# Kernel tuning notes

Measured on AMD Instinct MI355X. Metric: run time of the kernel, lower is better.

## Reference

```python
import jax, jax.numpy as jnp
import numpy as np

NU, NB, NI = 50000, 20000, 100000
D = 64
NUM_LAYERS = 2
CORE_K = 3
PAD = NI  # padding index for bundle_items
BATCH, NCAND = 2048, 2
MAXDEG = 50
E_UB, E_UI, E_BI = 800000, 1000000, 1200000
N_UB, N_UI, N_BI = NU + NB, NU + NI, NB + NI


def setup_inputs():
    key = jax.random.key(0)
    ks = jax.random.split(key, 24)
    f = jnp.float32
    inp = {
        'users_feature': jax.random.normal(ks[0], (NU, D), f) * 0.1,
        'bundles_feature': jax.random.normal(ks[1], (NB, D), f) * 0.1,
        'items_feature': jax.random.normal(ks[2], (NI, D), f) * 0.1,
        'mlp_core_w1': jax.random.normal(ks[3], (2, 32), f) * 0.1,
        'mlp_core_b1': jnp.zeros((32,), f),
        'mlp_core_w2': jax.random.normal(ks[4], (32, 1), f) * 0.1,
        'mlp_core_b2': jnp.zeros((1,), f),
        'mlp_syn_w1': jax.random.normal(ks[5], (2 * D, D), f) * 0.05,
        'mlp_syn_b1': jnp.zeros((D,), f),
        'mlp_syn_w2': jax.random.normal(ks[6], (D, D), f) * 0.05,
        'mlp_syn_b2': jnp.zeros((D,), f),
        'ub_val': jax.random.uniform(ks[7], (E_UB,), f) * 0.2,
        'ui_val': jax.random.uniform(ks[8], (E_UI,), f) * 0.2,
        'bi_val': jax.random.uniform(ks[9], (E_BI,), f) * 0.2,
        'users': jax.random.randint(ks[10], (BATCH,), 0, NU),
        'bundles': jax.random.randint(ks[11], (BATCH, NCAND), 0, NB),
        'ub_row': jax.random.randint(ks[12], (E_UB,), 0, N_UB, jnp.int32),
        'ub_col': jax.random.randint(ks[13], (E_UB,), 0, N_UB, jnp.int32),
        'ui_row': jax.random.randint(ks[14], (E_UI,), 0, N_UI, jnp.int32),
        'ui_col': jax.random.randint(ks[15], (E_UI,), 0, N_UI, jnp.int32),
        'bi_row': jax.random.randint(ks[16], (E_BI,), 0, N_BI, jnp.int32),
        'bi_col': jax.random.randint(ks[17], (E_BI,), 0, N_BI, jnp.int32),
        'bundle_items': jax.random.randint(ks[18], (NB, MAXDEG), 0, NI + 1),
    }
    return inp


def spmm(row, col, val, x):
    # y = A @ x for COO sparse A: gather source rows, scale, scatter-add to dest rows
    return jax.ops.segment_sum(val[:, None] * x[col], row, num_segments=x.shape[0])


def propagate(row, col, val, feat_a, feat_b):
    f = jnp.concatenate([feat_a, feat_b], axis=0)
    acc = f
    for _ in range(NUM_LAYERS):
        f = spmm(row, col, val, f)
        acc = acc + f
    m = acc / (NUM_LAYERS + 1)  # mean over hop outputs
    return m[:feat_a.shape[0]], m[feat_a.shape[0]:]


def core_fringe_scores(users, bundles, reps, bundle_items,
                       cw1, cb1, cw2, cb2, sw1, sb1, sw2, sb2):
    UB_u, UB_b, UI_u, UI_i, BI_b, BI_i = reps
    B, C = bundles.shape
    users_exp = jnp.repeat(users, C)            # [B*C]
    bundles_flat = bundles.reshape(-1)          # [B*C]
    bbi = bundle_items[bundles_flat]            # [B*C, M]
    mask = bbi != PAD
    zero = jnp.zeros((1, D), UI_i.dtype)
    items_ui = jnp.concatenate([UI_i, zero], 0)[bbi]  # [B*C, M, D]
    items_bi = jnp.concatenate([BI_i, zero], 0)[bbi]
    u_ui = UI_u[users_exp]                      # [B*C, D]
    b_bi = BI_b[bundles_flat]
    r_UI = jnp.einsum('nd,nmd->nm', u_ui, items_ui)
    r_BI = jnp.einsum('nd,nmd->nm', b_bi, items_bi)
    x = jnp.stack([r_UI, r_BI], axis=-1)        # [B*C, M, 2]
    h = jax.nn.relu(x @ cw1 + cb1)              # dropout omitted (eval-mode determinism)
    logits = (h @ cw2 + cb2)[..., 0]
    logits = jnp.where(mask, logits, -jnp.inf)
    pi = jax.nn.softmax(logits, axis=1)
    k = min(CORE_K, bbi.shape[1])
    topv, topi = jax.lax.top_k(pi, k)
    topp = topv / (topv.sum(axis=1, keepdims=True) + 1e-10)
    core_emb = jnp.take_along_axis(items_ui, topi[:, :, None], axis=1)
    h_core = (core_emb * topp[:, :, None]).sum(axis=1)
    n = pi.shape[0]
    is_core = jnp.zeros(pi.shape, bool).at[jnp.arange(n)[:, None], topi].set(True)
    is_fringe = mask & ~is_core
    fr = is_fringe[:, :, None].astype(items_ui.dtype)
    fringe_sum = (items_ui * fr).sum(axis=1)
    fringe_cnt = jnp.maximum(is_fringe.sum(axis=1, keepdims=True).astype(items_ui.dtype), 1.0)
    h_fringe = fringe_sum / fringe_cnt
    syn = jnp.concatenate([h_core, h_fringe], axis=1)
    phi = jax.nn.relu(syn @ sw1 + sb1) @ sw2 + sb2
    hat_e_BI = h_core + phi
    user_final = jnp.concatenate([u_ui, UB_u[users_exp]], axis=1)
    bundle_final = jnp.concatenate([UB_b[bundles_flat], hat_e_BI], axis=1)
    scores = (user_final * bundle_final).sum(axis=1)
    return scores.reshape(B, C)


def reference(users_feature, bundles_feature, items_feature,
              mlp_core_w1, mlp_core_b1, mlp_core_w2, mlp_core_b2,
              mlp_syn_w1, mlp_syn_b1, mlp_syn_w2, mlp_syn_b2,
              ub_val, ui_val, bi_val,
              users, bundles, ub_row, ub_col, ui_row, ui_col,
              bi_row, bi_col, bundle_items):
    UB_u, UB_b = propagate(ub_row, ub_col, ub_val, users_feature, bundles_feature)
    UI_u, UI_i = propagate(ui_row, ui_col, ui_val, users_feature, items_feature)
    BI_b, BI_i = propagate(bi_row, bi_col, bi_val, bundles_feature, items_feature)
    reps = (UB_u, UB_b, UI_u, UI_i, BI_b, BI_i)
    scores = core_fringe_scores(users, bundles, reps, bundle_items,
                                mlp_core_w1, mlp_core_b1, mlp_core_w2, mlp_core_b2,
                                mlp_syn_w1, mlp_syn_b1, mlp_syn_w2, mlp_syn_b2)
    # BPR loss: -log(sigmoid(pos - neg)) == softplus(neg - pos)
    bpr_loss = jnp.mean(jax.nn.softplus(scores[:, 1:] - scores[:, 0:1]))
    return bpr_loss
```

## Files before the change

### kernel.cpp

```cpp
#include <hip/hip_runtime.h>
#include <math.h>

constexpr int D = 64;
constexpr int NU = 50000, NB = 20000, NI = 100000;
constexpr int BATCH = 2048, NCAND = 2, MAXDEG = 50, CORE_K = 3;
constexpr int PAD_IDX = NI;
constexpr int N_UB = NU + NB, N_UI = NU + NI, N_BI = NB + NI;
constexpr int N_TOT = N_UB + N_UI + N_BI;
constexpr int OFF1 = N_UB;
constexpr int OFF2 = N_UB + N_UI;
constexpr int CAP = 48;
constexpr float VAL_SCALE = 16383.0f / 0.2f;
constexpr float VAL_INV   = 0.2f / 16383.0f;

constexpr int BSHIFT = 11;
constexpr int BROWS  = 1 << BSHIFT;
constexpr int NBUCK  = (N_TOT + BROWS - 1) >> BSHIFT;
constexpr int BCAP   = 28672;
constexpr int P1_EPT = 16;
constexpr int P1_TPB = 256;
constexpr int P1_EPB = P1_EPT * P1_TPB;

constexpr int L2_NCB = BATCH * NCAND;
constexpr int L2_SLOTS = 2 * NI + 2 * BATCH + 2 * L2_NCB;

__device__ __forceinline__ float wave_sum64(float v) {
#pragma unroll
    for (int off = 32; off > 0; off >>= 1) v += __shfl_down(v, off);
    return v;
}

__device__ __forceinline__ float bflo(unsigned u) { return __uint_as_float(u << 16); }
__device__ __forceinline__ float bfhi(unsigned u) { return __uint_as_float(u & 0xFFFF0000u); }
__device__ __forceinline__ unsigned short f2bf(float f) {
    unsigned u = __float_as_uint(f);
    u += 0x7FFF + ((u >> 16) & 1);
    return (unsigned short)(u >> 16);
}
__device__ __forceinline__ unsigned pack2(float a, float b) {
    return (unsigned)f2bf(a) | ((unsigned)f2bf(b) << 16);
}
__device__ __forceinline__ float bf1(const unsigned short* p) {
    return __uint_as_float(((unsigned)*p) << 16);
}

__global__ __launch_bounds__(256) void k_bin1(
    const int* __restrict__ r0, const int* __restrict__ c0,
    const float* __restrict__ v0,
    const int* __restrict__ r1, const int* __restrict__ c1,
    const float* __restrict__ v1,
    const int* __restrict__ r2, const int* __restrict__ c2,
    const float* __restrict__ v2,
    int e0, int e1, int e2,
    int* __restrict__ bcnt, uint2* __restrict__ stage) {
    __shared__ int s_hist[NBUCK];
    __shared__ unsigned s_base[NBUCK];
    const int t = threadIdx.x;
    const int etot = e0 + e1 + e2;
    const int i0 = blockIdx.x * P1_EPB + t;
    if (t < NBUCK) s_hist[t] = 0;
    __syncthreads();
    unsigned el[P1_EPT], er[P1_EPT];
#pragma unroll
    for (int k = 0; k < P1_EPT; ++k) {
        int i = i0 + k * P1_TPB;
        if (i < etot) {
            int r, c; float v;
            if (i < e0)           { r = r0[i];                 c = c0[i]; v = v0[i]; }
            else if (i < e0 + e1) { int j = i - e0;      r = r1[j] + OFF1; c = c1[j]; v = v1[j]; }
            else                  { int j = i - e0 - e1; r = r2[j] + OFF2; c = c2[j]; v = v2[j]; }
            unsigned q = (unsigned)fminf(v * VAL_SCALE + 0.5f, 16383.0f);
            el[k] = (q << 18) | (unsigned)c;
            int lo = atomicAdd(&s_hist[r >> BSHIFT], 1);
            er[k] = (unsigned)r | ((unsigned)lo << 19);
        } else {
            er[k] = 0xFFFFFFFFu;
        }
    }
    __syncthreads();
    if (t < NBUCK) s_base[t] = (unsigned)atomicAdd(&bcnt[t], s_hist[t]);
    __syncthreads();
#pragma unroll
    for (int k = 0; k < P1_EPT; ++k) {
        unsigned eh = er[k];
        if (eh == 0xFFFFFFFFu) continue;
        unsigned r = eh & 0x7FFFFu;
        unsigned b = r >> BSHIFT;
        unsigned slot = s_base[b] + (eh >> 19);
        if (slot < (unsigned)BCAP)
            stage[(size_t)b * BCAP + slot] = make_uint2(el[k], r);
    }
}

__global__ __launch_bounds__(1024) void k_bin2(
    const int* __restrict__ bcnt, const uint2* __restrict__ stage,
    int* __restrict__ cnt, unsigned* __restrict__ cv) {
    __shared__ int s_c[BROWS];
    const int b = blockIdx.x;
    const int t = threadIdx.x;
    for (int l = t; l < BROWS; l += 1024) s_c[l] = 0;
    __syncthreads();
    int nb = bcnt[b]; if (nb > BCAP) nb = BCAP;
    const uint2* sp = stage + (size_t)b * BCAP;
    const int rbase = b << BSHIFT;
    for (int i = t; i < nb; i += 1024) {
        uint2 e = sp[i];
        int r = (int)e.y;
        int slot = atomicAdd(&s_c[r - rbase], 1);
        if (slot < CAP) cv[(size_t)r * CAP + slot] = e.x;
    }
    __syncthreads();
    for (int l = t; l < BROWS; l += 1024) {
        int r = rbase + l;
        if (r < N_TOT) cnt[r] = s_c[l];
    }
}

__global__ __launch_bounds__(256) void k_cvt(const float* __restrict__ uf,
                                             const float* __restrict__ bf,
                                             const float* __restrict__ itf,
                                             unsigned short* __restrict__ xb) {
    size_t i = (size_t)blockIdx.x * 256 + threadIdx.x;
    if (i >= (size_t)N_TOT * 16) return;
    int row = (int)(i >> 4);
    int q = ((int)i & 15) * 4;
    const float* src;
    if (row < OFF1) {
        int l = row;
        src = (l < NU) ? uf + (size_t)l * D : bf + (size_t)(l - NU) * D;
    } else if (row < OFF2) {
        int l = row - OFF1;
        src = (l < NU) ? uf + (size_t)l * D : itf + (size_t)(l - NU) * D;
    } else {
        int l = row - OFF2;
        src = (l < NB) ? bf + (size_t)l * D : itf + (size_t)(l - NB) * D;
    }
    float4 v = *(const float4*)(src + q);
    ushort4 o;
    o.x = f2bf(v.x); o.y = f2bf(v.y); o.z = f2bf(v.z); o.w = f2bf(v.w);
    *(ushort4*)(xb + (size_t)row * D + q) = o;
}

__device__ __forceinline__ void edge_decode(unsigned u, int& col, float& v) {
    col = (int)(u & 0x3FFFFu);
    v = (float)(u >> 18) * VAL_INV;
}

__global__ __launch_bounds__(256) void k_spmm_l1(
    const int* __restrict__ cnt, const unsigned* __restrict__ cv,
    const unsigned short* __restrict__ xb, unsigned short* __restrict__ y1) {
    int r = blockIdx.x * 32 + (threadIdx.x >> 3);
    int t = threadIdx.x & 7;
    if (r >= N_TOT) return;
    int base = (r < OFF1) ? 0 : ((r < OFF2) ? OFF1 : OFF2);
    int deg = cnt[r]; if (deg > CAP) deg = CAP;
    const unsigned* ce = cv + (size_t)r * CAP;
    float a[8];
#pragma unroll
    for (int k = 0; k < 8; ++k) a[k] = 0.f;
    int j = 0;
    for (; j + 3 < deg; j += 4) {
        int c[4]; float v[4]; uint4 u[4];
#pragma unroll
        for (int k = 0; k < 4; ++k) edge_decode(ce[j + k], c[k], v[k]);
#pragma unroll
        for (int k = 0; k < 4; ++k)
            u[k] = *(const uint4*)(xb + (((size_t)(base + c[k])) << 6) + t * 8);
#pragma unroll
        for (int k = 0; k < 4; ++k) {
            a[0] = fmaf(v[k], bflo(u[k].x), a[0]); a[1] = fmaf(v[k], bfhi(u[k].x), a[1]);
            a[2] = fmaf(v[k], bflo(u[k].y), a[2]); a[3] = fmaf(v[k], bfhi(u[k].y), a[3]);
            a[4] = fmaf(v[k], bflo(u[k].z), a[4]); a[5] = fmaf(v[k], bfhi(u[k].z), a[5]);
            a[6] = fmaf(v[k], bflo(u[k].w), a[6]); a[7] = fmaf(v[k], bfhi(u[k].w), a[7]);
        }
    }
    for (; j < deg; ++j) {
        int c0; float v0;
        edge_decode(ce[j], c0, v0);
        uint4 u0 = *(const uint4*)(xb + (((size_t)(base + c0)) << 6) + t * 8);
        a[0] = fmaf(v0, bflo(u0.x), a[0]); a[1] = fmaf(v0, bfhi(u0.x), a[1]);
        a[2] = fmaf(v0, bflo(u0.y), a[2]); a[3] = fmaf(v0, bfhi(u0.y), a[3]);
        a[4] = fmaf(v0, bflo(u0.z), a[4]); a[5] = fmaf(v0, bfhi(u0.z), a[5]);
        a[6] = fmaf(v0, bflo(u0.w), a[6]); a[7] = fmaf(v0, bfhi(u0.w), a[7]);
    }
    uint4 o;
    o.x = pack2(a[0], a[1]); o.y = pack2(a[2], a[3]);
    o.z = pack2(a[4], a[5]); o.w = pack2(a[6], a[7]);
    *(uint4*)(y1 + ((size_t)r << 6) + t * 8) = o;
}

__global__ __launch_bounds__(256) void k_spmm_l2(
    const int* __restrict__ cnt, const unsigned* __restrict__ cv,
    const int* __restrict__ users, const int* __restrict__ bundles,
    const unsigned short* __restrict__ y1, unsigned short* __restrict__ xb) {
    int s = blockIdx.x * 32 + (threadIdx.x >> 3);
    int t = threadIdx.x & 7;
    if (s >= L2_SLOTS) return;
    int r;
    if (s < NI)                r = OFF1 + NU + s;
    else if (s < 2 * NI)       r = OFF2 + NB + (s - NI);
    else {
        int q = s - 2 * NI;
        if (q < BATCH)                 r = users[q];
        else if (q < 2 * BATCH)        r = OFF1 + users[q - BATCH];
        else if (q < 2 * BATCH + L2_NCB) r = NU + bundles[q - 2 * BATCH];
        else                           r = OFF2 + bundles[q - 2 * BATCH - L2_NCB];
    }
    int base = (r < OFF1) ? 0 : ((r < OFF2) ? OFF1 : OFF2);
    int deg = cnt[r]; if (deg > CAP) deg = CAP;
    const unsigned* ce = cv + (size_t)r * CAP;
    float a[8];
#pragma unroll
    for (int k = 0; k < 8; ++k) a[k] = 0.f;
    int j = 0;
    for (; j + 3 < deg; j += 4) {
        int c[4]; float v[4]; uint4 u[4];
#pragma unroll
        for (int k = 0; k < 4; ++k) edge_decode(ce[j + k], c[k], v[k]);
#pragma unroll
        for (int k = 0; k < 4; ++k)
            u[k] = *(const uint4*)(y1 + (((size_t)(base + c[k])) << 6) + t * 8);
#pragma unroll
        for (int k = 0; k < 4; ++k) {
            a[0] = fmaf(v[k], bflo(u[k].x), a[0]); a[1] = fmaf(v[k], bfhi(u[k].x), a[1]);
            a[2] = fmaf(v[k], bflo(u[k].y), a[2]); a[3] = fmaf(v[k], bfhi(u[k].y), a[3]);
            a[4] = fmaf(v[k], bflo(u[k].z), a[4]); a[5] = fmaf(v[k], bfhi(u[k].z), a[5]);
            a[6] = fmaf(v[k], bflo(u[k].w), a[6]); a[7] = fmaf(v[k], bfhi(u[k].w), a[7]);
        }
    }
    for (; j < deg; ++j) {
        int c0; float v0;
        edge_decode(ce[j], c0, v0);
        uint4 u0 = *(const uint4*)(y1 + (((size_t)(base + c0)) << 6) + t * 8);
        a[0] = fmaf(v0, bflo(u0.x), a[0]); a[1] = fmaf(v0, bfhi(u0.x), a[1]);
        a[2] = fmaf(v0, bflo(u0.y), a[2]); a[3] = fmaf(v0, bfhi(u0.y), a[3]);
        a[4] = fmaf(v0, bflo(u0.z), a[4]); a[5] = fmaf(v0, bfhi(u0.z), a[5]);
        a[6] = fmaf(v0, bflo(u0.w), a[6]); a[7] = fmaf(v0, bfhi(u0.w), a[7]);
    }
    uint4 fx = *(const uint4*)(xb + ((size_t)r << 6) + t * 8);
    uint4 yx = *(const uint4*)(y1 + ((size_t)r << 6) + t * 8);
    constexpr float k3 = 1.0f / 3.0f;
    float o[8];
    o[0] = (bflo(fx.x) + bflo(yx.x) + a[0]) * k3;
    o[1] = (bfhi(fx.x) + bfhi(yx.x) + a[1]) * k3;
    o[2] = (bflo(fx.y) + bflo(yx.y) + a[2]) * k3;
    o[3] = (bfhi(fx.y) + bfhi(yx.y) + a[3]) * k3;
    o[4] = (bflo(fx.z) + bflo(yx.z) + a[4]) * k3;
    o[5] = (bfhi(fx.z) + bfhi(yx.z) + a[5]) * k3;
    o[6] = (bflo(fx.w) + bflo(yx.w) + a[6]) * k3;
    o[7] = (bfhi(fx.w) + bfhi(yx.w) + a[7]) * k3;
    uint4 w;
    w.x = pack2(o[0], o[1]); w.y = pack2(o[2], o[3]);
    w.z = pack2(o[4], o[5]); w.w = pack2(o[6], o[7]);
    *(uint4*)(xb + ((size_t)r << 6) + t * 8) = w;
}

__global__ __launch_bounds__(256) void k_score(
    const int* __restrict__ users, const int* __restrict__ bundles,
    const int* __restrict__ bundle_items,
    const unsigned short* __restrict__ m_ub,
    const unsigned short* __restrict__ m_ui,
    const unsigned short* __restrict__ m_bi,
    const float* __restrict__ cw1, const float* __restrict__ cb1,
    const float* __restrict__ cw2, const float* __restrict__ cb2,
    const float* __restrict__ sw1, const float* __restrict__ sb1,
    const float* __restrict__ sw2, const float* __restrict__ sb2,
    float* __restrict__ scores) {
    const int t  = threadIdx.x;
    const int wv = t >> 6;
    const int ln = t & 63;
    const int n  = blockIdx.x * 4 + wv;
    const int g8 = ln >> 3;
    const int l8 = ln & 7;
    const int u = users[n >> 1];
    const int b = bundles[n];

    __shared__ unsigned sh_it[4][MAXDEG][32];
    __shared__ float sh_r[4][2][MAXDEG];
    __shared__ float sh_syn[4][2 * D];
    __shared__ float sh_h1[4][D];

    int my_idx = (ln < MAXDEG) ? bundle_items[(size_t)b * MAXDEG + ln] : PAD_IDX;
    unsigned long long vmask = __ballot(my_idx != PAD_IDX);

    uint4 ufr = *(const uint4*)(m_ui + ((size_t)u << 6) + l8 * 8);
    uint4 bfr = *(const uint4*)(m_bi + ((size_t)b << 6) + l8 * 8);
    float uf0 = bflo(ufr.x), uf1 = bfhi(ufr.x), uf2 = bflo(ufr.y), uf3 = bfhi(ufr.y);
    float uf4 = bflo(ufr.z), uf5 = bfhi(ufr.z), uf6 = bflo(ufr.w), uf7 = bfhi(ufr.w);
    float bf0 = bflo(bfr.x), bf1_ = bfhi(bfr.x), bf2 = bflo(bfr.y), bf3 = bfhi(bfr.y);
    float bf4 = bflo(bfr.z), bf5 = bfhi(bfr.z), bf6 = bflo(bfr.w), bf7 = bfhi(bfr.w);

    for (int iter = 0; iter < (MAXDEG + 7) / 8; ++iter) {
        int m = iter * 8 + g8;
        if (m >= MAXDEG) continue;
        int it = __shfl(my_idx, m);
        uint4 iu = make_uint4(0, 0, 0, 0);
        float pu = 0.f, pb = 0.f;
        if (it != PAD_IDX) {
            iu = *(const uint4*)(m_ui + ((size_t)(NU + it) << 6) + l8 * 8);
            uint4 ib = *(const uint4*)(m_bi + ((size_t)(NB + it) << 6) + l8 * 8);
            pu = uf0 * bflo(iu.x) + uf1 * bfhi(iu.x) + uf2 * bflo(iu.y) + uf3 * bfhi(iu.y)
               + uf4 * bflo(iu.z) + uf5 * bfhi(iu.z) + uf6 * bflo(iu.w) + uf7 * bfhi(iu.w);
            pb = bf0 * bflo(ib.x) + bf1_ * bfhi(ib.x) + bf2 * bflo(ib.y) + bf3 * bfhi(ib.y)
               + bf4 * bflo(ib.z) + bf5 * bfhi(ib.z) + bf6 * bflo(ib.w) + bf7 * bfhi(ib.w);
        }
        *(uint4*)&sh_it[wv][m][l8 * 4] = iu;
#pragma unroll
        for (int off = 4; off > 0; off >>= 1) {
            pu += __shfl_down(pu, off, 8);
            pb += __shfl_down(pb, off, 8);
        }
        if (l8 == 0) { sh_r[wv][0][m] = pu; sh_r[wv][1][m] = pb; }
    }
    __builtin_amdgcn_wave_barrier();

    float logit = -INFINITY;
    if (ln < MAXDEG && my_idx != PAD_IDX) {
        float rU = sh_r[wv][0][ln], rB = sh_r[wv][1][ln];
        float acc = cb2[0];
#pragma unroll
        for (int j = 0; j < 32; ++j) {
            float h = fmaf(rU, cw1[j], fmaf(rB, cw1[32 + j], cb1[j]));
            h = fmaxf(h, 0.f);
            acc = fmaf(h, cw2[j], acc);
        }
        logit = acc;
    }

    float mx = logit;
#pragma unroll
    for (int off = 32; off > 0; off >>= 1) mx = fmaxf(mx, __shfl_xor(mx, off));
    float e = expf(logit - mx);
    float sm = e;
#pragma unroll
    for (int off = 32; off > 0; off >>= 1) sm += __shfl_xor(sm, off);
    float p = e / sm;

    int ti[CORE_K]; float tp[CORE_K];
    float vsel = p;
#pragma unroll
    for (int k = 0; k < CORE_K; ++k) {
        float vv = vsel; int ii = ln;
#pragma unroll
        for (int off = 32; off > 0; off >>= 1) {
            float v2 = __shfl_xor(vv, off);
            int   i2 = __shfl_xor(ii, off);
            if (v2 > vv || (v2 == vv && i2 < ii)) { vv = v2; ii = i2; }
        }
        ti[k] = ii; tp[k] = vv;
        if (ln == ii) vsel = -1.f;
    }
    float tinv = 1.f / (tp[0] + tp[1] + tp[2] + 1e-10f);
    tp[0] *= tinv; tp[1] *= tinv; tp[2] *= tinv;

    int ti0 = ti[0], ti1 = ti[1], ti2 = ti[2];
    const int ui_w = ln >> 1;
    const bool hi = (ln & 1);
    auto feat = [&](int m) -> float {
        unsigned w = sh_it[wv][m][ui_w];
        return hi ? bfhi(w) : bflo(w);
    };
    float hcore = feat(ti0) * tp[0] + feat(ti1) * tp[1] + feat(ti2) * tp[2];
    float fsum = 0.f;
#pragma unroll 10
    for (int m = 0; m < MAXDEG; ++m) fsum += feat(m);
    int fcnt = __popcll(vmask);
#pragma unroll
    for (int k = 0; k < CORE_K; ++k) {
        if ((vmask >> ti[k]) & 1ull) { fsum -= feat(ti[k]); fcnt--; }
    }
    float hfr = fsum / fmaxf((float)fcnt, 1.f);
    sh_syn[wv][ln] = hcore;
    sh_syn[wv][D + ln] = hfr;
    __builtin_amdgcn_wave_barrier();

    float h1 = sb1[ln];
#pragma unroll 8
    for (int k0 = 0; k0 < 32; ++k0) {
        float4 s4 = *(const float4*)&sh_syn[wv][k0 * 4];
        h1 = fmaf(s4.x, sw1[(k0 * 4 + 0) * D + ln], h1);
        h1 = fmaf(s4.y, sw1[(k0 * 4 + 1) * D + ln], h1);
        h1 = fmaf(s4.z, sw1[(k0 * 4 + 2) * D + ln], h1);
        h1 = fmaf(s4.w, sw1[(k0 * 4 + 3) * D + ln], h1);
    }
    sh_h1[wv][ln] = fmaxf(h1, 0.f);
    __builtin_amdgcn_wave_barrier();
    float phi = sb2[ln];
#pragma unroll 8
    for (int k0 = 0; k0 < 16; ++k0) {
        float4 s4 = *(const float4*)&sh_h1[wv][k0 * 4];
        phi = fmaf(s4.x, sw2[(k0 * 4 + 0) * D + ln], phi);
        phi = fmaf(s4.y, sw2[(k0 * 4 + 1) * D + ln], phi);
        phi = fmaf(s4.z, sw2[(k0 * 4 + 2) * D + ln], phi);
        phi = fmaf(s4.w, sw2[(k0 * 4 + 3) * D + ln], phi);
    }

    float hat = hcore + phi;
    float uui = bf1(m_ui + ((size_t)u << 6) + ln);
    float ubu = bf1(m_ub + ((size_t)u << 6) + ln);
    float ubb = bf1(m_ub + ((size_t)(NU + b) << 6) + ln);
    float part = wave_sum64(uui * ubb + ubu * hat);
    if (ln == 0) scores[n] = part;
}

__global__ __launch_bounds__(256) void k_loss(const float* __restrict__ scores,
                                              float* __restrict__ out) {
    __shared__ float red[256];
    float s = 0.f;
    for (int i = threadIdx.x; i < BATCH; i += 256) {
        float x = scores[i * 2 + 1] - scores[i * 2 + 0];
        s += fmaxf(x, 0.f) + log1pf(expf(-fabsf(x)));
    }
    red[threadIdx.x] = s;
    __syncthreads();
    for (int w = 128; w > 0; w >>= 1) {
        if (threadIdx.x < w) red[threadIdx.x] += red[threadIdx.x + w];
        __syncthreads();
    }
    if (threadIdx.x == 0) out[0] = red[0] / (float)BATCH;
}

extern "C" void kernel_launch(void* const* d_in, const int* in_sizes, int n_in,
                              void* d_out, int out_size, void* d_ws, size_t ws_size,
                              hipStream_t stream) {
    const float* users_feature   = (const float*)d_in[0];
    const float* bundles_feature = (const float*)d_in[1];
    const float* items_feature   = (const float*)d_in[2];
    const float* cw1 = (const float*)d_in[3];
    const float* cb1 = (const float*)d_in[4];
    const float* cw2 = (const float*)d_in[5];
    const float* cb2 = (const float*)d_in[6];
    const float* sw1 = (const float*)d_in[7];
    const float* sb1 = (const float*)d_in[8];
    const float* sw2 = (const float*)d_in[9];
    const float* sb2 = (const float*)d_in[10];
    const float* ub_val = (const float*)d_in[11];
    const float* ui_val = (const float*)d_in[12];
    const float* bi_val = (const float*)d_in[13];
    const int* users   = (const int*)d_in[14];
    const int* bundles = (const int*)d_in[15];
    const int* ub_row = (const int*)d_in[16];
    const int* ub_col = (const int*)d_in[17];
    const int* ui_row = (const int*)d_in[18];
    const int* ui_col = (const int*)d_in[19];
    const int* bi_row = (const int*)d_in[20];
    const int* bi_col = (const int*)d_in[21];
    const int* bundle_items = (const int*)d_in[22];
    const int E_UB = in_sizes[11], E_UI = in_sizes[12], E_BI = in_sizes[13];
    const int E_TOT = E_UB + E_UI + E_BI;

    float* ws = (float*)d_ws;
    size_t off = 0;
    unsigned short* xb  = (unsigned short*)(ws + off); off += (size_t)N_TOT * 32;
    unsigned short* y1b = (unsigned short*)(ws + off); off += (size_t)N_TOT * 32;
    float* scores = ws + off; off += (size_t)BATCH * NCAND;
    int*   cnt    = (int*)(ws + off); off += N_TOT;
    unsigned* cv  = (unsigned*)(ws + off); off += (size_t)N_TOT * CAP;
    int*   bcnt   = (int*)(ws + off); off += NBUCK;
    if (ws_size < off * sizeof(float)) return;

    uint2* stage = (uint2*)y1b;

    hipMemsetAsync(bcnt, 0, NBUCK * sizeof(int), stream);
    k_bin1<<<(E_TOT + P1_EPB - 1) / P1_EPB, P1_TPB, 0, stream>>>(
        ub_row, ub_col, ub_val, ui_row, ui_col, ui_val, bi_row, bi_col, bi_val,
        E_UB, E_UI, E_BI, bcnt, stage);
    k_bin2<<<NBUCK, 1024, 0, stream>>>(bcnt, stage, cnt, cv);

    k_cvt<<<(int)(((size_t)N_TOT * 16 + 255) / 256), 256, 0, stream>>>(
        users_feature, bundles_feature, items_feature, xb);
    int sb1blocks = (N_TOT + 31) / 32;
    k_spmm_l1<<<sb1blocks, 256, 0, stream>>>(cnt, cv, xb, y1b);
    int sb2blocks = (L2_SLOTS + 31) / 32;
    k_spmm_l2<<<sb2blocks, 256, 0, stream>>>(cnt, cv, users, bundles, y1b, xb);

    k_score<<<(BATCH * NCAND) / 4, 256, 0, stream>>>(
        users, bundles, bundle_items,
        xb, xb + (size_t)OFF1 * D, xb + (size_t)OFF2 * D,
        cw1, cb1, cw2, cb2, sw1, sb1, sw2, sb2, scores);

    k_loss<<<1, 256, 0, stream>>>(scores, (float*)d_out);
}
```

Before: 362.7 us.

## Deduplicate bf16 feature table and write compact layer-2 outputs indexed by slot

The bf16 conversion now writes a single deduplicated table of users, bundles and items instead of one copy per graph. Edge columns are remapped to global feature indices at binning time, so layer-1 gathers read this smaller table, which should improve cache reuse and cut conversion traffic. Layer-2 writes its results to a compact slot-indexed buffer that the scoring kernel reads directly. The cost is extra index remapping logic in the layer-2 gather path.

```diff
diff --git a/kernel.cpp b/kernel.cpp
--- a/kernel.cpp
+++ b/kernel.cpp
@@ -13,6 +13,10 @@
 constexpr float VAL_SCALE = 16383.0f / 0.2f;
 constexpr float VAL_INV   = 0.2f / 16383.0f;
 
+constexpr int GB_BASE = NU;
+constexpr int GI_BASE = NU + NB;
+constexpr int NGF = NU + NB + NI;
+
 constexpr int BSHIFT = 11;
 constexpr int BROWS  = 1 << BSHIFT;
 constexpr int NBUCK  = (N_TOT + BROWS - 1) >> BSHIFT;
@@ -23,6 +27,10 @@
 
 constexpr int L2_NCB = BATCH * NCAND;
 constexpr int L2_SLOTS = 2 * NI + 2 * BATCH + 2 * L2_NCB;
+constexpr int S_UBU = 2 * NI;
+constexpr int S_UIU = 2 * NI + BATCH;
+constexpr int S_UBB = 2 * NI + 2 * BATCH;
+constexpr int S_BIB = S_UBB + L2_NCB;
 
 __device__ __forceinline__ float wave_sum64(float v) {
 #pragma unroll
@@ -65,12 +73,14 @@
     for (int k = 0; k < P1_EPT; ++k) {
         int i = i0 + k * P1_TPB;
         if (i < etot) {
-            int r, c; float v;
-            if (i < e0)           { r = r0[i];                 c = c0[i]; v = v0[i]; }
-            else if (i < e0 + e1) { int j = i - e0;      r = r1[j] + OFF1; c = c1[j]; v = v1[j]; }
-            else                  { int j = i - e0 - e1; r = r2[j] + OFF2; c = c2[j]; v = v2[j]; }
+            int r, g; float v;
+            if (i < e0)           { r = r0[i]; g = c0[i]; v = v0[i]; }
+            else if (i < e0 + e1) { int j = i - e0; r = r1[j] + OFF1;
+                                    int c = c1[j]; g = (c < NU) ? c : c + NB; v = v1[j]; }
+            else                  { int j = i - e0 - e1; r = r2[j] + OFF2;
+                                    g = c2[j] + NU; v = v2[j]; }
             unsigned q = (unsigned)fminf(v * VAL_SCALE + 0.5f, 16383.0f);
-            el[k] = (q << 18) | (unsigned)c;
+            el[k] = (q << 18) | (unsigned)g;
             int lo = atomicAdd(&s_hist[r >> BSHIFT], 1);
             er[k] = (unsigned)r | ((unsigned)lo << 19);
         } else {
@@ -119,26 +129,19 @@
 __global__ __launch_bounds__(256) void k_cvt(const float* __restrict__ uf,
                                              const float* __restrict__ bf,
                                              const float* __restrict__ itf,
-                                             unsigned short* __restrict__ xb) {
+                                             unsigned short* __restrict__ gt) {
     size_t i = (size_t)blockIdx.x * 256 + threadIdx.x;
-    if (i >= (size_t)N_TOT * 16) return;
+    if (i >= (size_t)NGF * 16) return;
     int row = (int)(i >> 4);
     int q = ((int)i & 15) * 4;
     const float* src;
-    if (row < OFF1) {
-        int l = row;
-        src = (l < NU) ? uf + (size_t)l * D : bf + (size_t)(l - NU) * D;
-    } else if (row < OFF2) {
-        int l = row - OFF1;
-        src = (l < NU) ? uf + (size_t)l * D : itf + (size_t)(l - NU) * D;
-    } else {
-        int l = row - OFF2;
-        src = (l < NB) ? bf + (size_t)l * D : itf + (size_t)(l - NB) * D;
-    }
+    if (row < GB_BASE)      src = uf  + (size_t)row * D;
+    else if (row < GI_BASE) src = bf  + (size_t)(row - GB_BASE) * D;
+    else                    src = itf + (size_t)(row - GI_BASE) * D;
     float4 v = *(const float4*)(src + q);
     ushort4 o;
     o.x = f2bf(v.x); o.y = f2bf(v.y); o.z = f2bf(v.z); o.w = f2bf(v.w);
-    *(ushort4*)(xb + (size_t)row * D + q) = o;
+    *(ushort4*)(gt + (size_t)row * D + q) = o;
 }
 
 __device__ __forceinline__ void edge_decode(unsigned u, int& col, float& v) {
@@ -148,11 +151,10 @@
 
 __global__ __launch_bounds__(256) void k_spmm_l1(
     const int* __restrict__ cnt, const unsigned* __restrict__ cv,
-    const unsigned short* __restrict__ xb, unsigned short* __restrict__ y1) {
+    const unsigned short* __restrict__ gt, unsigned short* __restrict__ y1) {
     int r = blockIdx.x * 32 + (threadIdx.x >> 3);
     int t = threadIdx.x & 7;
     if (r >= N_TOT) return;
-    int base = (r < OFF1) ? 0 : ((r < OFF2) ? OFF1 : OFF2);
     int deg = cnt[r]; if (deg > CAP) deg = CAP;
     const unsigned* ce = cv + (size_t)r * CAP;
     float a[8];
@@ -165,7 +167,7 @@
         for (int k = 0; k < 4; ++k) edge_decode(ce[j + k], c[k], v[k]);
 #pragma unroll
         for (int k = 0; k < 4; ++k)
-            u[k] = *(const uint4*)(xb + (((size_t)(base + c[k])) << 6) + t * 8);
+            u[k] = *(const uint4*)(gt + (((size_t)c[k]) << 6) + t * 8);
 #pragma unroll
         for (int k = 0; k < 4; ++k) {
             a[0] = fmaf(v[k], bflo(u[k].x), a[0]); a[1] = fmaf(v[k], bfhi(u[k].x), a[1]);
@@ -177,7 +179,7 @@
     for (; j < deg; ++j) {
         int c0; float v0;
         edge_decode(ce[j], c0, v0);
-        uint4 u0 = *(const uint4*)(xb + (((size_t)(base + c0)) << 6) + t * 8);
+        uint4 u0 = *(const uint4*)(gt + (((size_t)c0) << 6) + t * 8);
         a[0] = fmaf(v0, bflo(u0.x), a[0]); a[1] = fmaf(v0, bfhi(u0.x), a[1]);
         a[2] = fmaf(v0, bflo(u0.y), a[2]); a[3] = fmaf(v0, bfhi(u0.y), a[3]);
         a[4] = fmaf(v0, bflo(u0.z), a[4]); a[5] = fmaf(v0, bfhi(u0.z), a[5]);
@@ -192,21 +194,29 @@
 __global__ __launch_bounds__(256) void k_spmm_l2(
     const int* __restrict__ cnt, const unsigned* __restrict__ cv,
     const int* __restrict__ users, const int* __restrict__ bundles,
-    const unsigned short* __restrict__ y1, unsigned short* __restrict__ xb) {
+    const unsigned short* __restrict__ y1, const unsigned short* __restrict__ gt,
+    unsigned short* __restrict__ xc) {
     int s = blockIdx.x * 32 + (threadIdx.x >> 3);
     int t = threadIdx.x & 7;
     if (s >= L2_SLOTS) return;
-    int r;
-    if (s < NI)                r = OFF1 + NU + s;
-    else if (s < 2 * NI)       r = OFF2 + NB + (s - NI);
+    int r, g, sec;
+    if (s < NI)                { r = OFF1 + NU + s;        g = GI_BASE + s;        sec = 1; }
+    else if (s < 2 * NI)       { int i = s - NI;
+                                 r = OFF2 + NB + i;        g = GI_BASE + i;        sec = 2; }
     else {
         int q = s - 2 * NI;
-        if (q < BATCH)                 r = users[q];
-        else if (q < 2 * BATCH)        r = OFF1 + users[q - BATCH];
-        else if (q < 2 * BATCH + L2_NCB) r = NU + bundles[q - 2 * BATCH];
-        else                           r = OFF2 + bundles[q - 2 * BATCH - L2_NCB];
-    }
-    int base = (r < OFF1) ? 0 : ((r < OFF2) ? OFF1 : OFF2);
+        if (q < BATCH)            { int u = users[q];             r = u;         g = u;            sec = 0; }
+        else if (q < 2 * BATCH)   { int u = users[q - BATCH];     r = OFF1 + u;  g = u;            sec = 1; }
+        else if (q < S_BIB - 2 * NI) { int b = bundles[q - 2 * BATCH];
+                                    r = NU + b;    g = GB_BASE + b;  sec = 0; }
+        else                      { int b = bundles[q - (S_BIB - 2 * NI)];
+                                    r = OFF2 + b;  g = GB_BASE + b;  sec = 2; }
+    }
+    auto y1row = [&](int gg) -> int {
+        if (sec == 0) return gg;
+        if (sec == 2) return OFF2 - GB_BASE + gg;
+        return OFF1 + ((gg < NU) ? gg : gg - NB);
+    };
     int deg = cnt[r]; if (deg > CAP) deg = CAP;
     const unsigned* ce = cv + (size_t)r * CAP;
     float a[8];
@@ -219,7 +229,7 @@
         for (int k = 0; k < 4; ++k) edge_decode(ce[j + k], c[k], v[k]);
 #pragma unroll
         for (int k = 0; k < 4; ++k)
-            u[k] = *(const uint4*)(y1 + (((size_t)(base + c[k])) << 6) + t * 8);
+            u[k] = *(const uint4*)(y1 + (((size_t)y1row(c[k])) << 6) + t * 8);
 #pragma unroll
         for (int k = 0; k < 4; ++k) {
             a[0] = fmaf(v[k], bflo(u[k].x), a[0]); a[1] = fmaf(v[k], bfhi(u[k].x), a[1]);
@@ -231,13 +241,13 @@
     for (; j < deg; ++j) {
         int c0; float v0;
         edge_decode(ce[j], c0, v0);
-        uint4 u0 = *(const uint4*)(y1 + (((size_t)(base + c0)) << 6) + t * 8);
+        uint4 u0 = *(const uint4*)(y1 + (((size_t)y1row(c0)) << 6) + t * 8);
         a[0] = fmaf(v0, bflo(u0.x), a[0]); a[1] = fmaf(v0, bfhi(u0.x), a[1]);
         a[2] = fmaf(v0, bflo(u0.y), a[2]); a[3] = fmaf(v0, bfhi(u0.y), a[3]);
         a[4] = fmaf(v0, bflo(u0.z), a[4]); a[5] = fmaf(v0, bfhi(u0.z), a[5]);
         a[6] = fmaf(v0, bflo(u0.w), a[6]); a[7] = fmaf(v0, bfhi(u0.w), a[7]);
     }
-    uint4 fx = *(const uint4*)(xb + ((size_t)r << 6) + t * 8);
+    uint4 fx = *(const uint4*)(gt + ((size_t)g << 6) + t * 8);
     uint4 yx = *(const uint4*)(y1 + ((size_t)r << 6) + t * 8);
     constexpr float k3 = 1.0f / 3.0f;
     float o[8];
@@ -252,15 +262,13 @@
     uint4 w;
     w.x = pack2(o[0], o[1]); w.y = pack2(o[2], o[3]);
     w.z = pack2(o[4], o[5]); w.w = pack2(o[6], o[7]);
-    *(uint4*)(xb + ((size_t)r << 6) + t * 8) = w;
+    *(uint4*)(xc + ((size_t)s << 6) + t * 8) = w;
 }
 
 __global__ __launch_bounds__(256) void k_score(
-    const int* __restrict__ users, const int* __restrict__ bundles,
+    const int* __restrict__ bundles,
     const int* __restrict__ bundle_items,
-    const unsigned short* __restrict__ m_ub,
-    const unsigned short* __restrict__ m_ui,
-    const unsigned short* __restrict__ m_bi,
+    const unsigned short* __restrict__ xc,
     const float* __restrict__ cw1, const float* __restrict__ cb1,
     const float* __restrict__ cw2, const float* __restrict__ cb2,
     const float* __restrict__ sw1, const float* __restrict__ sb1,
@@ -272,7 +280,7 @@
     const int n  = blockIdx.x * 4 + wv;
     const int g8 = ln >> 3;
     const int l8 = ln & 7;
-    const int u = users[n >> 1];
+    const int uq = n >> 1;
     const int b = bundles[n];
 
     __shared__ unsigned sh_it[4][MAXDEG][32];
@@ -283,8 +291,8 @@
     int my_idx = (ln < MAXDEG) ? bundle_items[(size_t)b * MAXDEG + ln] : PAD_IDX;
     unsigned long long vmask = __ballot(my_idx != PAD_IDX);
 
-    uint4 ufr = *(const uint4*)(m_ui + ((size_t)u << 6) + l8 * 8);
-    uint4 bfr = *(const uint4*)(m_bi + ((size_t)b << 6) + l8 * 8);
+    uint4 ufr = *(const uint4*)(xc + (((size_t)(S_UIU + uq)) << 6) + l8 * 8);
+    uint4 bfr = *(const uint4*)(xc + (((size_t)(S_BIB + n)) << 6) + l8 * 8);
     float uf0 = bflo(ufr.x), uf1 = bfhi(ufr.x), uf2 = bflo(ufr.y), uf3 = bfhi(ufr.y);
     float uf4 = bflo(ufr.z), uf5 = bfhi(ufr.z), uf6 = bflo(ufr.w), uf7 = bfhi(ufr.w);
     float bf0 = bflo(bfr.x), bf1_ = bfhi(bfr.x), bf2 = bflo(bfr.y), bf3 = bfhi(bfr.y);
@@ -297,8 +305,8 @@
         uint4 iu = make_uint4(0, 0, 0, 0);
         float pu = 0.f, pb = 0.f;
         if (it != PAD_IDX) {
-            iu = *(const uint4*)(m_ui + ((size_t)(NU + it) << 6) + l8 * 8);
-            uint4 ib = *(const uint4*)(m_bi + ((size_t)(NB + it) << 6) + l8 * 8);
+            iu = *(const uint4*)(xc + (((size_t)it) << 6) + l8 * 8);
+            uint4 ib = *(const uint4*)(xc + (((size_t)(NI + it)) << 6) + l8 * 8);
             pu = uf0 * bflo(iu.x) + uf1 * bfhi(iu.x) + uf2 * bflo(iu.y) + uf3 * bfhi(iu.y)
                + uf4 * bflo(iu.z) + uf5 * bfhi(iu.z) + uf6 * bflo(iu.w) + uf7 * bfhi(iu.w);
             pb = bf0 * bflo(ib.x) + bf1_ * bfhi(ib.x) + bf2 * bflo(ib.y) + bf3 * bfhi(ib.y)
@@ -396,9 +404,9 @@
     }
 
     float hat = hcore + phi;
-    float uui = bf1(m_ui + ((size_t)u << 6) + ln);
-    float ubu = bf1(m_ub + ((size_t)u << 6) + ln);
-    float ubb = bf1(m_ub + ((size_t)(NU + b) << 6) + ln);
+    float uui = bf1(xc + (((size_t)(S_UIU + uq)) << 6) + ln);
+    float ubu = bf1(xc + (((size_t)(S_UBU + uq)) << 6) + ln);
+    float ubb = bf1(xc + (((size_t)(S_UBB + n)) << 6) + ln);
     float part = wave_sum64(uui * ubb + ubu * hat);
     if (ln == 0) scores[n] = part;
 }
@@ -451,7 +459,8 @@
 
     float* ws = (float*)d_ws;
     size_t off = 0;
-    unsigned short* xb  = (unsigned short*)(ws + off); off += (size_t)N_TOT * 32;
+    unsigned short* gt  = (unsigned short*)(ws + off); off += (size_t)NGF * 32;
+    unsigned short* xc  = (unsigned short*)(ws + off); off += (size_t)L2_SLOTS * 32;
     unsigned short* y1b = (unsigned short*)(ws + off); off += (size_t)N_TOT * 32;
     float* scores = ws + off; off += (size_t)BATCH * NCAND;
     int*   cnt    = (int*)(ws + off); off += N_TOT;
@@ -467,16 +476,15 @@
         E_UB, E_UI, E_BI, bcnt, stage);
     k_bin2<<<NBUCK, 1024, 0, stream>>>(bcnt, stage, cnt, cv);
 
-    k_cvt<<<(int)(((size_t)N_TOT * 16 + 255) / 256), 256, 0, stream>>>(
-        users_feature, bundles_feature, items_feature, xb);
+    k_cvt<<<(int)(((size_t)NGF * 16 + 255) / 256), 256, 0, stream>>>(
+        users_feature, bundles_feature, items_feature, gt);
     int sb1blocks = (N_TOT + 31) / 32;
-    k_spmm_l1<<<sb1blocks, 256, 0, stream>>>(cnt, cv, xb, y1b);
+    k_spmm_l1<<<sb1blocks, 256, 0, stream>>>(cnt, cv, gt, y1b);
     int sb2blocks = (L2_SLOTS + 31) / 32;
-    k_spmm_l2<<<sb2blocks, 256, 0, stream>>>(cnt, cv, users, bundles, y1b, xb);
+    k_spmm_l2<<<sb2blocks, 256, 0, stream>>>(cnt, cv, users, bundles, y1b, gt, xc);
 
     k_score<<<(BATCH * NCAND) / 4, 256, 0, stream>>>(
-        users, bundles, bundle_items,
-        xb, xb + (size_t)OFF1 * D, xb + (size_t)OFF2 * D,
+        bundles, bundle_items, xc,
         cw1, cb1, cw2, cb2, sw1, sb1, sw2, sb2, scores);
 
     k_loss<<<1, 256, 0, stream>>>(scores, (float*)d_out);
```

After: 355.2 us. -2.1%, faster.
